# Kernel tuning notes

Measured on AMD Instinct MI355X. Metric: run time of the kernel, lower is better.

## Reference

```python
import jax, jax.numpy as jnp
from jax import lax
import numpy as np

N_NODES = 512
BATCH = 256
N_STEPS = 200
DT = 0.02  # t_span spacing; keeps 200 RK4 steps numerically tame


def setup_inputs() -> dict:
    key = jax.random.key(0)
    ks = jax.random.split(key, 7)
    s = 1.0 / np.sqrt(N_NODES)
    x_init = jax.random.normal(ks[0], (BATCH, N_NODES), dtype=jnp.float32)
    t_span = jnp.arange(N_STEPS, dtype=jnp.float32) * DT
    # MaskedLinear params (kaiming-uniform-ish scale)
    W1 = jax.random.uniform(ks[1], (N_NODES, N_NODES), jnp.float32, -s, s)
    b1 = jax.random.uniform(ks[2], (N_NODES,), jnp.float32, -s, s)
    # inner Linear params
    W2 = jax.random.uniform(ks[3], (N_NODES, N_NODES), jnp.float32, -s, s)
    b2 = jax.random.uniform(ks[4], (N_NODES,), jnp.float32, -s, s)
    mask = jax.random.bernoulli(ks[5], 0.1, (N_NODES, N_NODES)).astype(jnp.float32)
    mask = mask * (1.0 - jnp.eye(N_NODES, dtype=jnp.float32))
    return {"x_init": x_init, "t_span": t_span, "W1": W1, "b1": b1,
            "W2": W2, "b2": b2, "mask": mask}


def reference(x_init, t_span, W1, b1, W2, b2, mask):
    # ODE func: dydt = W2 @ tanh(masked(W1) @ y + b1) + b2 (t unused)
    Wm = W1 * mask  # [N, N]
    def f(y):  # y: [B, N]
        return jnp.tanh(y @ Wm.T + b1) @ W2.T + b2

    dts = t_span[1:] - t_span[:-1]  # [T-1]

    def rk4_step(y, dt):
        k1 = f(y)
        k2 = f(y + dt * k1 / 2)
        k3 = f(y + dt * k2 / 2)
        k4 = f(y + dt * k3)
        y_new = y + dt / 6 * (k1 + 2 * k2 + 2 * k3 + k4)
        return y_new, y_new

    _, traj = lax.scan(rk4_step, x_init, dts)  # [T-1, B, N]
    traj = jnp.concatenate([x_init[None], traj], axis=0)  # [T, B, N]
    return jnp.transpose(traj, (1, 0, 2))  # [B, T, N]
```

## Files before the change

kernel.cpp:

```cpp
#include <hip/hip_runtime.h>
#include <math.h>

#define NN 512
#define NB 256
#define NT 200
#define TPB 256
#define NTEAM 8

typedef unsigned long long u64;
typedef _Float16 half8 __attribute__((ext_vector_type(8)));
typedef float f32x4 __attribute__((ext_vector_type(4)));

#define WS_WM  0
#define WS_WC  (NN*NN)
#define WS_C   (WS_WC + NN*NN/2)
#define WS_X0  (WS_C + NN)
#define WS_HB0 (WS_X0 + NB*NN)
#define WS_CNT (WS_HB0 + NB*NN/2)

__device__ __forceinline__ void sysst_u64(u64* p, u64 v) {
  __hip_atomic_store(p, v, __ATOMIC_RELAXED, __HIP_MEMORY_SCOPE_SYSTEM);
}
__device__ __forceinline__ u64 sysld_u64(const u64* p) {
  return __hip_atomic_load(p, __ATOMIC_RELAXED, __HIP_MEMORY_SCOPE_SYSTEM);
}
__device__ __forceinline__ void sysst_f1(float* p, float v) {
  __hip_atomic_store(p, v, __ATOMIC_RELAXED, __HIP_MEMORY_SCOPE_SYSTEM);
}
__device__ __forceinline__ float sysld_f1(const float* p) {
  return __hip_atomic_load(p, __ATOMIC_RELAXED, __HIP_MEMORY_SCOPE_SYSTEM);
}
__device__ __forceinline__ void sysst_u16(unsigned short* p, unsigned short v) {
  __hip_atomic_store(p, v, __ATOMIC_RELAXED, __HIP_MEMORY_SCOPE_SYSTEM);
}
__device__ __forceinline__ void sysst_h(_Float16* p, float v) {
  union { _Float16 hf; unsigned short us; } cv; cv.hf = (_Float16)v;
  sysst_u16((unsigned short*)p, cv.us);
}

__global__ __launch_bounds__(256)
void k_init(const float* __restrict__ W1, const float* __restrict__ mask,
            const float* __restrict__ x_init, float* __restrict__ ws,
            float* __restrict__ out) {
  int gt = blockIdx.x * 256 + threadIdx.x;
  int stride = gridDim.x * 256;
  for (int i = gt; i < NN * NN; i += stride) ws[WS_WM + i] = W1[i] * mask[i];
  for (int i = gt; i < NB * NN / 2; i += stride) {
    u64 q = ((const u64*)x_init)[i];
    int r = i >> 8, np = i & 255;
    *((u64*)(out + (size_t)r * NT * NN) + np) = q;
  }
  if (gt < 32 * NTEAM * 16)
    __hip_atomic_store(((unsigned*)(ws + WS_CNT)) + gt, 0u,
                       __ATOMIC_RELAXED, __HIP_MEMORY_SCOPE_SYSTEM);
}

__global__ __launch_bounds__(128)
void k_prep(const float* __restrict__ W2g, const float* __restrict__ b2,
            const float* __restrict__ x_init, float* __restrict__ ws) {
  __shared__ float w1row[NN];
  const int j = blockIdx.x;
  const int t = threadIdx.x;
  const float* wm = ws + WS_WM + (size_t)j * NN;
  for (int i = t; i < NN; i += 128) w1row[i] = wm[i];
  __syncthreads();

  f32x4 acc = {0.f, 0.f, 0.f, 0.f};
  for (int m = 0; m < NN; ++m) {
    float w = w1row[m];
    if (w != 0.f)
      acc += w * ((const f32x4*)(W2g + (size_t)m * NN))[t];
  }
  _Float16* wcrow = (_Float16*)(ws + WS_WC) + (size_t)j * NN;
#pragma unroll
  for (int e = 0; e < 4; ++e) wcrow[4 * t + e] = (_Float16)acc[e];

  if (t == 0) {
    float s = 0.f;
    for (int m = 0; m < NN; ++m)
      if (w1row[m] != 0.f) s += b2[m] * w1row[m];
    ws[WS_C + j] = s;
  }

#pragma unroll
  for (int rr = 0; rr < 2; ++rr) {
    int r = t + rr * 128;
    const float* y0 = x_init + (size_t)r * NN;
    float s = 0.f;
    for (int m = 0; m < NN; ++m) {
      float w = w1row[m];
      if (w != 0.f) s = fmaf(y0[m], w, s);
    }
    sysst_f1(ws + WS_X0 + (size_t)r * NN + j, s);
  }
}

__device__ __forceinline__ void team_wait(unsigned* flagsp, unsigned target) {
  if (threadIdx.x < NTEAM) {
    while (__hip_atomic_load(flagsp + threadIdx.x * 16, __ATOMIC_RELAXED,
                             __HIP_MEMORY_SCOPE_AGENT) < target)
      __builtin_amdgcn_s_sleep(1);
  }
  __syncthreads();
}
__device__ __forceinline__ void team_release(unsigned* flagsp, int cg, unsigned e) {
  __syncthreads();
  if (threadIdx.x == 0)
    __hip_atomic_store(flagsp + cg * 16, e, __ATOMIC_RELAXED,
                       __HIP_MEMORY_SCOPE_SYSTEM);
}

struct St { u64 a0, a1, a2, a3; };
__device__ __forceinline__ St stage_load(const _Float16* __restrict__ src,
                                         int tid) {
  const int row = tid >> 5;
  const int seg = tid & 31;
  const u64* s = (const u64*)(src + (size_t)row * NN) + seg * 4;
  St v;
  v.a0 = sysld_u64(s);     v.a1 = sysld_u64(s + 1);
  v.a2 = sysld_u64(s + 2); v.a3 = sysld_u64(s + 3);
  return v;
}
__device__ __forceinline__ void stage_write(_Float16* __restrict__ plane,
                                            const St& v, int tid) {
  const int row = tid >> 5;
  const int seg = tid & 31;
  union { u64 q[2]; half8 h; } u0, u1;
  u0.q[0] = v.a0; u0.q[1] = v.a1; u1.q[0] = v.a2; u1.q[1] = v.a3;
  ((half8*)plane)[row * 64 + ((seg * 2) ^ row)] = u0.h;
  ((half8*)plane)[row * 64 + ((seg * 2 + 1) ^ row)] = u1.h;
}

__device__ __forceinline__ void gemm8(const _Float16* plane, const _Float16* wb,
                                      int rc, int kg, int wv, float res[4]) {
  const int swz = rc & 7;
  const half8* pA = (const half8*)plane;
  const half8* pB = (const half8*)wb;
  const int abase = (rc & 7) * 64;
  const int bbase = (wv * 16 + rc) * 64;
  f32x4 ae = {0.f, 0.f, 0.f, 0.f};
  f32x4 ao = {0.f, 0.f, 0.f, 0.f};
#pragma unroll
  for (int kt = 0; kt < 16; kt += 2) {
    const int g0 = (kt * 4 + kg) ^ swz;
    const int g1 = ((kt + 1) * 4 + kg) ^ swz;
    ae = __builtin_amdgcn_mfma_f32_16x16x32_f16(pA[abase + g0], pB[bbase + g0],
                                                ae, 0, 0, 0);
    ao = __builtin_amdgcn_mfma_f32_16x16x32_f16(pA[abase + g1], pB[bbase + g1],
                                                ao, 0, 0, 0);
  }
#pragma unroll
  for (int r = 0; r < 4; ++r) res[r] = ae[r] + ao[r];
}

__global__ __launch_bounds__(TPB, 1)
void k_ode(const float* __restrict__ tspan,
           const float* __restrict__ W2g,
           const float* __restrict__ b1,
           const float* __restrict__ b2,
           float* __restrict__ ws,
           float* __restrict__ out,
           const float* __restrict__ x_init) {
  extern __shared__ _Float16 ldsh[];
  _Float16* wc  = ldsh;
  _Float16* w2  = ldsh + 32768;
  _Float16* plA = ldsh + 65536;
  _Float16* plB = ldsh + 69632;

  const int bid = blockIdx.x;
  const int cg = bid & 7, rgA = bid >> 3;
  const int r0p[2] = {rgA * 8, rgA * 8 + 128};
  const int j0 = cg * 64;
  const int tid = threadIdx.x;
  const int lane = tid & 63, wv = tid >> 6;
  const int rc = lane & 15, kg = lane >> 4;
  const int mycol = j0 + wv * 16 + rc;
  const bool act = (kg < 2);

  unsigned* flbase = (unsigned*)(ws + WS_CNT);
  unsigned* flp[2] = {flbase + rgA * (NTEAM * 16),
                      flbase + (rgA + 16) * (NTEAM * 16)};
  _Float16* hb[2] = {(_Float16*)(ws + WS_HB0), (_Float16*)(ws + WS_WM)};

  {
    const int col = tid >> 2;
    const int part = tid & 3;
    const half8* s1 = (const half8*)((const _Float16*)(ws + WS_WC)
                                     + (size_t)(j0 + col) * NN) + part * 16;
    const float* s2 = W2g + (size_t)(j0 + col) * NN + part * 128;
    half8* d1 = (half8*)wc;
    half8* d2 = (half8*)w2;
    const int key = col & 7;
#pragma unroll
    for (int i = 0; i < 16; ++i) {
      int g = part * 16 + i;
      int idx = col * 64 + (g ^ key);
      d1[idx] = s1[i];
      half8 hv;
#pragma unroll
      for (int e = 0; e < 8; ++e) hv[e] = (_Float16)s2[i * 8 + e];
      d2[idx] = hv;
    }
  }
  const float b1s = b1[mycol], b2s = b2[mycol];
  const float c_own = ws[WS_C + mycol];

  float xb[2][4], yb[2][4], H[2][4];
  if (act) {
#pragma unroll
    for (int p = 0; p < 2; ++p)
#pragma unroll
      for (int r = 0; r < 4; ++r) {
        int row = r0p[p] + kg * 4 + r;
        xb[p][r] = sysld_f1(ws + WS_X0 + (size_t)row * NN + mycol);
        yb[p][r] = x_init[(size_t)row * NN + mycol];
        float h = tanhf(xb[p][r] + b1s);
        H[p][r] = h;
        sysst_h(hb[0] + (size_t)row * NN + mycol, h);
      }
  }
  __syncthreads();
  if (tid == 0) {
    __hip_atomic_store(flp[0] + cg * 16, 1u, __ATOMIC_RELAXED,
                       __HIP_MEMORY_SCOPE_SYSTEM);
    __hip_atomic_store(flp[1] + cg * 16, 1u, __ATOMIC_RELAXED,
                       __HIP_MEMORY_SCOPE_SYSTEM);
  }

  float res[4], res2[4];

  for (int t = 0; t < NT - 1; ++t) {
    const float dt = tspan[t + 1] - tspan[t];
    const float c6 = dt / 6.0f;
#pragma unroll 1
    for (int s = 0; s < 4; ++s) {
      const int q = t * 4 + s;
      const unsigned target = (unsigned)(q + 1);
      const _Float16* rdb = hb[q & 1];
      _Float16* wrb = hb[(q + 1) & 1];

      team_wait(flp[0], target);
      St va = stage_load(rdb + (size_t)r0p[0] * NN, tid);
      team_wait(flp[1], target);
      St vb = stage_load(rdb + (size_t)r0p[1] * NN, tid);

      stage_write(plA, va, tid);
      __syncthreads();
      gemm8(plA, wc, rc, kg, wv, res);
      if (s == 3) gemm8(plA, w2, rc, kg, wv, res2);
#pragma unroll
      for (int p = 0; p < 1; ++p) {}
      if (act) {
        if (s < 3) {
          const float a = (s == 2) ? dt : dt * 0.5f;
#pragma unroll
          for (int r = 0; r < 4; ++r) {
            float xs = xb[0][r] + a * (res[r] + c_own);
            float h = tanhf(xs + b1s);
            float st;
            if (s == 2) { H[0][r] += h;       st = H[0][r]; }
            else        { H[0][r] += 2.f * h; st = h;       }
            sysst_h(wrb + (size_t)(r0p[0] + kg * 4 + r) * NN + mycol, st);
          }
        } else {
#pragma unroll
          for (int r = 0; r < 4; ++r) {
            int row = r0p[0] + kg * 4 + r;
            xb[0][r] += c6 * res[r] + dt * c_own;
            yb[0][r] += c6 * res2[r] + dt * b2s;
            out[((size_t)row * NT + (t + 1)) * NN + mycol] = yb[0][r];
            float h = tanhf(xb[0][r] + b1s);
            H[0][r] = h;
            sysst_h(wrb + (size_t)row * NN + mycol, h);
          }
        }
      }
      team_release(flp[0], cg, target + 1);

      stage_write(plB, vb, tid);
      __syncthreads();
      gemm8(plB, wc, rc, kg, wv, res);
      if (s == 3) gemm8(plB, w2, rc, kg, wv, res2);
      if (act) {
        if (s < 3) {
          const float a = (s == 2) ? dt : dt * 0.5f;
#pragma unroll
          for (int r = 0; r < 4; ++r) {
            float xs = xb[1][r] + a * (res[r] + c_own);
            float h = tanhf(xs + b1s);
            float st;
            if (s == 2) { H[1][r] += h;       st = H[1][r]; }
            else        { H[1][r] += 2.f * h; st = h;       }
            sysst_h(wrb + (size_t)(r0p[1] + kg * 4 + r) * NN + mycol, st);
          }
        } else {
#pragma unroll
          for (int r = 0; r < 4; ++r) {
            int row = r0p[1] + kg * 4 + r;
            xb[1][r] += c6 * res[r] + dt * c_own;
            yb[1][r] += c6 * res2[r] + dt * b2s;
            out[((size_t)row * NT + (t + 1)) * NN + mycol] = yb[1][r];
            float h = tanhf(xb[1][r] + b1s);
            H[1][r] = h;
            sysst_h(wrb + (size_t)row * NN + mycol, h);
          }
        }
      }
      team_release(flp[1], cg, target + 1);
    }
  }
}

extern "C" void kernel_launch(void* const* d_in, const int* in_sizes, int n_in,
                              void* d_out, int out_size, void* d_ws, size_t ws_size,
                              hipStream_t stream) {
  const float* x_init = (const float*)d_in[0];
  const float* tspan  = (const float*)d_in[1];
  const float* W1     = (const float*)d_in[2];
  const float* b1     = (const float*)d_in[3];
  const float* W2     = (const float*)d_in[4];
  const float* b2     = (const float*)d_in[5];
  const float* mask   = (const float*)d_in[6];
  float* out = (float*)d_out;
  float* ws  = (float*)d_ws;

  hipLaunchKernelGGL(k_init, dim3(256), dim3(256), 0, stream,
                     W1, mask, x_init, ws, out);
  hipLaunchKernelGGL(k_prep, dim3(512), dim3(128), 0, stream,
                     W2, b2, x_init, ws);

  const unsigned ldsBytes = 144 * 1024;
  (void)hipFuncSetAttribute((const void*)k_ode,
                            hipFuncAttributeMaxDynamicSharedMemorySize,
                            (int)ldsBytes);

  hipLaunchKernelGGL(k_ode, dim3(128), dim3(TPB), ldsBytes, stream,
                     tspan, W2, b1, b2, ws, out, x_init);
}
```

Measured before the change: 2.925 ms.

## Halve rows per block and double persistent ODE grid to 256 blocks

The batch rows are split more finely: each block now handles 4 rows per half instead of 8, and the grid doubles from 128 to 256 persistent blocks. The staging load/write, the MFMA A-operand swizzle and the team flag layout are all rewritten to match. The aim is to spread the per-step GEMM and tanh work across more CUs and shorten the per-stage critical path. The cost is that only one of the four k-groups does useful row work, which wastes MFMA lanes, and there are more blocks to keep in spin-flag sync. All blocks must still be co-resident for the flag scheme to work.

```diff
diff --git a/kernel.cpp b/kernel.cpp
--- a/kernel.cpp
+++ b/kernel.cpp
@@ -50,7 +50,7 @@
     int r = i >> 8, np = i & 255;
     *((u64*)(out + (size_t)r * NT * NN) + np) = q;
   }
-  if (gt < 32 * NTEAM * 16)
+  if (gt < 64 * NTEAM * 16)
     __hip_atomic_store(((unsigned*)(ws + WS_CNT)) + gt, 0u,
                        __ATOMIC_RELAXED, __HIP_MEMORY_SCOPE_SYSTEM);
 }
@@ -110,43 +110,42 @@
                        __HIP_MEMORY_SCOPE_SYSTEM);
 }
 
-struct St { u64 a0, a1, a2, a3; };
+struct St { u64 a0, a1; };
 __device__ __forceinline__ St stage_load(const _Float16* __restrict__ src,
                                          int tid) {
-  const int row = tid >> 5;
-  const int seg = tid & 31;
-  const u64* s = (const u64*)(src + (size_t)row * NN) + seg * 4;
-  St v;
-  v.a0 = sysld_u64(s);     v.a1 = sysld_u64(s + 1);
-  v.a2 = sysld_u64(s + 2); v.a3 = sysld_u64(s + 3);
+  const int row = tid >> 6;
+  const int g = tid & 63;
+  const u64* s = (const u64*)(src + (size_t)row * NN) + g * 2;
+  St v; v.a0 = sysld_u64(s); v.a1 = sysld_u64(s + 1);
   return v;
 }
 __device__ __forceinline__ void stage_write(_Float16* __restrict__ plane,
                                             const St& v, int tid) {
-  const int row = tid >> 5;
-  const int seg = tid & 31;
-  union { u64 q[2]; half8 h; } u0, u1;
-  u0.q[0] = v.a0; u0.q[1] = v.a1; u1.q[0] = v.a2; u1.q[1] = v.a3;
-  ((half8*)plane)[row * 64 + ((seg * 2) ^ row)] = u0.h;
-  ((half8*)plane)[row * 64 + ((seg * 2 + 1) ^ row)] = u1.h;
+  const int row = tid >> 6;
+  const int g = tid & 63;
+  union { u64 q[2]; half8 h; } u; u.q[0] = v.a0; u.q[1] = v.a1;
+  ((half8*)plane)[row * 64 + (g ^ row)] = u.h;
 }
 
 __device__ __forceinline__ void gemm8(const _Float16* plane, const _Float16* wb,
                                       int rc, int kg, int wv, float res[4]) {
-  const int swz = rc & 7;
+  const int swzA = rc & 3;
+  const int swzB = rc & 7;
   const half8* pA = (const half8*)plane;
   const half8* pB = (const half8*)wb;
-  const int abase = (rc & 7) * 64;
+  const int abase = (rc & 3) * 64;
   const int bbase = (wv * 16 + rc) * 64;
   f32x4 ae = {0.f, 0.f, 0.f, 0.f};
   f32x4 ao = {0.f, 0.f, 0.f, 0.f};
 #pragma unroll
   for (int kt = 0; kt < 16; kt += 2) {
-    const int g0 = (kt * 4 + kg) ^ swz;
-    const int g1 = ((kt + 1) * 4 + kg) ^ swz;
-    ae = __builtin_amdgcn_mfma_f32_16x16x32_f16(pA[abase + g0], pB[bbase + g0],
+    const int k0 = kt * 4 + kg;
+    const int k1 = (kt + 1) * 4 + kg;
+    ae = __builtin_amdgcn_mfma_f32_16x16x32_f16(pA[abase + (k0 ^ swzA)],
+                                                pB[bbase + (k0 ^ swzB)],
                                                 ae, 0, 0, 0);
-    ao = __builtin_amdgcn_mfma_f32_16x16x32_f16(pA[abase + g1], pB[bbase + g1],
+    ao = __builtin_amdgcn_mfma_f32_16x16x32_f16(pA[abase + (k1 ^ swzA)],
+                                                pB[bbase + (k1 ^ swzB)],
                                                 ao, 0, 0, 0);
   }
 #pragma unroll
@@ -165,21 +164,21 @@
   _Float16* wc  = ldsh;
   _Float16* w2  = ldsh + 32768;
   _Float16* plA = ldsh + 65536;
-  _Float16* plB = ldsh + 69632;
+  _Float16* plB = ldsh + 67584;
 
   const int bid = blockIdx.x;
   const int cg = bid & 7, rgA = bid >> 3;
-  const int r0p[2] = {rgA * 8, rgA * 8 + 128};
+  const int r0p[2] = {rgA * 4, rgA * 4 + 128};
   const int j0 = cg * 64;
   const int tid = threadIdx.x;
   const int lane = tid & 63, wv = tid >> 6;
   const int rc = lane & 15, kg = lane >> 4;
   const int mycol = j0 + wv * 16 + rc;
-  const bool act = (kg < 2);
+  const bool act = (kg == 0);
 
   unsigned* flbase = (unsigned*)(ws + WS_CNT);
   unsigned* flp[2] = {flbase + rgA * (NTEAM * 16),
-                      flbase + (rgA + 16) * (NTEAM * 16)};
+                      flbase + (rgA + 32) * (NTEAM * 16)};
   _Float16* hb[2] = {(_Float16*)(ws + WS_HB0), (_Float16*)(ws + WS_WM)};
 
   {
@@ -211,7 +210,7 @@
     for (int p = 0; p < 2; ++p)
 #pragma unroll
       for (int r = 0; r < 4; ++r) {
-        int row = r0p[p] + kg * 4 + r;
+        int row = r0p[p] + r;
         xb[p][r] = sysld_f1(ws + WS_X0 + (size_t)row * NN + mycol);
         yb[p][r] = x_init[(size_t)row * NN + mycol];
         float h = tanhf(xb[p][r] + b1s);
@@ -248,8 +247,6 @@
       __syncthreads();
       gemm8(plA, wc, rc, kg, wv, res);
       if (s == 3) gemm8(plA, w2, rc, kg, wv, res2);
-#pragma unroll
-      for (int p = 0; p < 1; ++p) {}
       if (act) {
         if (s < 3) {
           const float a = (s == 2) ? dt : dt * 0.5f;
@@ -260,12 +257,12 @@
             float st;
             if (s == 2) { H[0][r] += h;       st = H[0][r]; }
             else        { H[0][r] += 2.f * h; st = h;       }
-            sysst_h(wrb + (size_t)(r0p[0] + kg * 4 + r) * NN + mycol, st);
+            sysst_h(wrb + (size_t)(r0p[0] + r) * NN + mycol, st);
           }
         } else {
 #pragma unroll
           for (int r = 0; r < 4; ++r) {
-            int row = r0p[0] + kg * 4 + r;
+            int row = r0p[0] + r;
             xb[0][r] += c6 * res[r] + dt * c_own;
             yb[0][r] += c6 * res2[r] + dt * b2s;
             out[((size_t)row * NT + (t + 1)) * NN + mycol] = yb[0][r];
@@ -291,12 +288,12 @@
             float st;
             if (s == 2) { H[1][r] += h;       st = H[1][r]; }
             else        { H[1][r] += 2.f * h; st = h;       }
-            sysst_h(wrb + (size_t)(r0p[1] + kg * 4 + r) * NN + mycol, st);
+            sysst_h(wrb + (size_t)(r0p[1] + r) * NN + mycol, st);
           }
         } else {
 #pragma unroll
           for (int r = 0; r < 4; ++r) {
-            int row = r0p[1] + kg * 4 + r;
+            int row = r0p[1] + r;
             xb[1][r] += c6 * res[r] + dt * c_own;
             yb[1][r] += c6 * res2[r] + dt * b2s;
             out[((size_t)row * NT + (t + 1)) * NN + mycol] = yb[1][r];
@@ -329,11 +326,11 @@
   hipLaunchKernelGGL(k_prep, dim3(512), dim3(128), 0, stream,
                      W2, b2, x_init, ws);
 
-  const unsigned ldsBytes = 144 * 1024;
+  const unsigned ldsBytes = 136 * 1024;
   (void)hipFuncSetAttribute((const void*)k_ode,
                             hipFuncAttributeMaxDynamicSharedMemorySize,
                             (int)ldsBytes);
 
-  hipLaunchKernelGGL(k_ode, dim3(128), dim3(TPB), ldsBytes, stream,
+  hipLaunchKernelGGL(k_ode, dim3(256), dim3(TPB), ldsBytes, stream,
                      tspan, W2, b1, b2, ws, out, x_init);
 }
```

Result: faster. 2.668 ms (-8.8%).
